# Kernel tuning notes

Measured on AMD Instinct MI355X. Metric: run time of the kernel, lower is better.

Reference implementation:

```python
import jax, jax.numpy as jnp
import numpy as np

EPS = 1e-16

def _householder_cascade(vectors):
    # vectors: [N, S, 1]
    v = vectors[..., 0]                                  # [N, S]
    outer = jnp.einsum('ns,nt->nst', v, v)               # [N, S, S]
    inner = jnp.sum(v * v, axis=-1)[:, None, None]       # [N, 1, 1]
    S = v.shape[-1]
    I = jnp.eye(S, dtype=vectors.dtype)
    hh = I[None] - 2.0 * outer / (inner + EPS)           # [N, S, S]
    # sequential left-to-right product: Q = H_0 @ H_1 @ ... @ H_{N-1}
    def step(Q, M):
        return Q @ M, None
    Q, _ = jax.lax.scan(step, I, hh)
    return Q

def setup_inputs() -> dict:
    key = jax.random.key(0)
    k1, k2 = jax.random.split(key)
    S, N, B = 256, 258, 65536
    vectors = jax.random.normal(k1, (N, S, 1), dtype=jnp.float32)
    vectors = vectors / jnp.linalg.norm(vectors, axis=1, keepdims=True)
    x = jax.random.normal(k2, (B, S), dtype=jnp.float32)
    return {"x": x, "vectors": vectors}

def reference(x, vectors):
    Q = _householder_cascade(vectors)   # [S, S]
    return x @ Q.T
```

## Files before the change

kernel.cpp:

```cpp
#include <hip/hip_runtime.h>


#define GLOAD_LDS16(g, l)                                                      \
  __builtin_amdgcn_global_load_lds(                                            \
      (const __attribute__((address_space(1))) void*)(g),                      \
      (__attribute__((address_space(3))) void*)(l), 16, 0, 0)

typedef __attribute__((ext_vector_type(8))) short bf16x8;
typedef __attribute__((ext_vector_type(4))) float f32x4;

__device__ __forceinline__ unsigned short f2bf_rne(float f) {
  unsigned u = __builtin_bit_cast(unsigned, f);
  return (unsigned short)((u + 0x7fffu + ((u >> 16) & 1u)) >> 16);
}

template <int CTRL>
__device__ __forceinline__ float dpp_add(float v) {
  int t = __builtin_amdgcn_update_dpp(0, __builtin_bit_cast(int, v), CTRL, 0xF,
                                      0xF, true);
  return v + __builtin_bit_cast(float, t);
}

__device__ __forceinline__ float dpp_sum16(float p) {
  p = dpp_add<0xB1>(p);
  p = dpp_add<0x4E>(p);
  p = dpp_add<0x124>(p);
  p = dpp_add<0x128>(p);
  return p;
}

__launch_bounds__(64, 1)
__global__ void hh_qchunk(const float* __restrict__ vecs,
                          float* __restrict__ Qc) {
  const int l = threadIdx.x;
  const int chunk = blockIdx.x >> 6;
  const int rg = blockIdx.x & 63;
  const int r = l >> 4;
  const int cl = l & 15;
  const int row = rg * 4 + r;
  const int col0 = cl * 16;
  const int brow = chunk * 129;

  __shared__ float cs[132];

  for (int n = r; n < 129; n += 4) {
    const f32x4* vp = (const f32x4*)(vecs + (long)(brow + n) * 256 + col0);
    float s = 0.f;
#pragma unroll
    for (int i = 0; i < 4; ++i) {
      f32x4 t = vp[i];
      s += t[0] * t[0] + t[1] * t[1] + t[2] * t[2] + t[3] * t[3];
    }
    s = dpp_sum16(s);
    if (cl == 0) cs[n] = 2.0f / (s + 1e-16f);
  }
  if (l < 3) cs[129 + l] = 0.f;
  __syncthreads();

  float q[16];
#pragma unroll
  for (int i = 0; i < 16; ++i) q[i] = (col0 + i == row) ? 1.f : 0.f;

  auto load16 = [&](float(&d)[16], int n) {
    int gr = brow + n;
    gr = gr > 257 ? 257 : gr;
    const float4* v = (const float4*)(vecs + (long)gr * 256 + col0);
#pragma unroll
    for (int i = 0; i < 4; ++i) {
      float4 t = v[i];
      d[4 * i] = t.x; d[4 * i + 1] = t.y; d[4 * i + 2] = t.z; d[4 * i + 3] = t.w;
    }
  };

  auto step = [&](const float(&a)[16], float cc) {
    float p0 = 0.f, p1 = 0.f, p2 = 0.f, p3 = 0.f;
#pragma unroll
    for (int e = 0; e < 4; ++e) {
      p0 = fmaf(q[e], a[e], p0);
      p1 = fmaf(q[4 + e], a[4 + e], p1);
      p2 = fmaf(q[8 + e], a[8 + e], p2);
      p3 = fmaf(q[12 + e], a[12 + e], p3);
    }
    const float p = dpp_sum16((p0 + p1) + (p2 + p3));
    const float s = cc * p;
#pragma unroll
    for (int k = 0; k < 16; ++k) q[k] = fmaf(-s, a[k], q[k]);
  };

  float A0[16], A1[16];
  load16(A0, 0);
  load16(A1, 1);
  float c0 = cs[0], c1 = cs[1];
  for (int n = 0; n < 128; n += 2) {
    const float cn0 = cs[n + 2], cn1 = cs[n + 3];
    step(A0, c0);
    load16(A0, n + 2);
    step(A1, c1);
    load16(A1, n + 3);
    c0 = cn0; c1 = cn1;
  }
  step(A0, c0);

  float4* out = (float4*)(Qc + (long)chunk * 65536 + row * 256 + col0);
#pragma unroll
  for (int i = 0; i < 4; ++i)
    out[i] = make_float4(q[4 * i], q[4 * i + 1], q[4 * i + 2], q[4 * i + 3]);
}

__launch_bounds__(256)
__global__ void hh_mm(const float* __restrict__ in,
                      unsigned short* __restrict__ outb) {
  const int t = blockIdx.x;
  const int ti = (t >> 3) * 32, tj = (t & 7) * 32;
  const int tid = threadIdx.x;
  const int tx = tid & 15, ty = tid >> 4;
  const float* A = in;
  const float* Bm = in + 65536;

  __shared__ float As[32][68];
  __shared__ float Bs[64][36];

  float acc00 = 0.f, acc01 = 0.f, acc10 = 0.f, acc11 = 0.f;

  for (int k0 = 0; k0 < 256; k0 += 64) {
#pragma unroll
    for (int u0 = 0; u0 < 2048; u0 += 1024) {
      int idx = u0 + tid * 4;
      int rr = idx >> 6, cc = idx & 63;
      *(float4*)&As[rr][cc] = *(const float4*)&A[(ti + rr) * 256 + k0 + cc];
      int kk = idx >> 5, jj = idx & 31;
      *(float4*)&Bs[kk][jj] = *(const float4*)&Bm[(k0 + kk) * 256 + tj + jj];
    }
    __syncthreads();
#pragma unroll 8
    for (int kk = 0; kk < 64; ++kk) {
      float a0 = As[2 * ty][kk], a1 = As[2 * ty + 1][kk];
      float b0 = Bs[kk][2 * tx], b1 = Bs[kk][2 * tx + 1];
      acc00 = fmaf(a0, b0, acc00);
      acc01 = fmaf(a0, b1, acc01);
      acc10 = fmaf(a1, b0, acc10);
      acc11 = fmaf(a1, b1, acc11);
    }
    __syncthreads();
  }

  const int gi = ti + 2 * ty, gj = tj + 2 * tx;
  outb[gi * 256 + gj] = f2bf_rne(acc00);
  outb[gi * 256 + gj + 1] = f2bf_rne(acc01);
  outb[(gi + 1) * 256 + gj] = f2bf_rne(acc10);
  outb[(gi + 1) * 256 + gj + 1] = f2bf_rne(acc11);
}

__launch_bounds__(512)
__global__ void hh_gemm(const float* __restrict__ X,
                        const unsigned short* __restrict__ Qb,
                        float* __restrict__ Y) {
  __shared__ __align__(128) char lds[65536];
  const int tid = threadIdx.x;
  const int lane = tid & 63;
  const int wid = tid >> 6;
  const int wm = wid >> 2;
  const int wn = wid & 3;
  const int fr = lane & 15;
  const int fg = lane >> 4;
  const long bm0 = (long)blockIdx.x * 128;

  auto stage = [&](int buf, int kt) {
#pragma unroll
    for (int r2 = 0; r2 < 2; ++r2) {
      int slot = r2 * 512 + tid;
      int row = slot >> 3, seg = slot & 7;
      int ps = seg ^ (row & 7);
      GLOAD_LDS16(X + (bm0 + row) * 256 + kt * 32 + ps * 4,
                  lds + buf * 16384 + slot * 16);
    }
#pragma unroll
    for (int r2 = 0; r2 < 2; ++r2) {
      int slot = r2 * 512 + tid;
      int row = slot >> 2, seg = slot & 3;
      int ps = seg ^ (row & 3);
      GLOAD_LDS16(Qb + row * 256 + kt * 32 + ps * 8,
                  lds + 32768 + buf * 16384 + slot * 16);
    }
  };

  f32x4 acc[4][4];
#pragma unroll
  for (int m = 0; m < 4; ++m)
#pragma unroll
    for (int n = 0; n < 4; ++n) acc[m][n] = (f32x4){0.f, 0.f, 0.f, 0.f};

  stage(0, 0);
  __syncthreads();

  for (int kt = 0; kt < 8; ++kt) {
    const int cur = kt & 1;
    if (kt < 7) stage(cur ^ 1, kt + 1);

    bf16x8 aF[4], bF[4];
#pragma unroll
    for (int m = 0; m < 4; ++m) {
      int row = wm * 64 + m * 16 + fr;
      int s0 = (2 * fg) ^ (row & 7);
      int s1 = (2 * fg + 1) ^ (row & 7);
      const f32x4 x0 = *(const f32x4*)(lds + cur * 16384 + row * 128 + s0 * 16);
      const f32x4 x1 = *(const f32x4*)(lds + cur * 16384 + row * 128 + s1 * 16);
      bf16x8 t;
      t[0] = (short)f2bf_rne(x0[0]);
      t[1] = (short)f2bf_rne(x0[1]);
      t[2] = (short)f2bf_rne(x0[2]);
      t[3] = (short)f2bf_rne(x0[3]);
      t[4] = (short)f2bf_rne(x1[0]);
      t[5] = (short)f2bf_rne(x1[1]);
      t[6] = (short)f2bf_rne(x1[2]);
      t[7] = (short)f2bf_rne(x1[3]);
      aF[m] = t;
    }
#pragma unroll
    for (int n = 0; n < 4; ++n) {
      int row = wn * 64 + n * 16 + fr;
      int ps = fg ^ (row & 3);
      bF[n] = *(const bf16x8*)(lds + 32768 + cur * 16384 + row * 64 + ps * 16);
    }
#pragma unroll
    for (int m = 0; m < 4; ++m)
#pragma unroll
      for (int n = 0; n < 4; ++n)
        acc[m][n] =
            __builtin_amdgcn_mfma_f32_16x16x32_bf16(aF[m], bF[n], acc[m][n], 0, 0, 0);
    __syncthreads();
  }

#pragma unroll
  for (int m = 0; m < 4; ++m)
#pragma unroll
    for (int n = 0; n < 4; ++n)
#pragma unroll
      for (int r = 0; r < 4; ++r) {
        long grow = bm0 + wm * 64 + m * 16 + fg * 4 + r;
        int gcol = wn * 64 + n * 16 + fr;
        Y[grow * 256 + gcol] = acc[m][n][r];
      }
}

extern "C" void kernel_launch(void* const* d_in, const int* in_sizes, int n_in,
                              void* d_out, int out_size, void* d_ws, size_t ws_size,
                              hipStream_t stream) {
  const float* x = (const float*)d_in[0];
  const float* vecs = (const float*)d_in[1];
  float* y = (float*)d_out;

  unsigned short* Qb = (unsigned short*)d_ws;
  float* Qc = (float*)d_out;

  hh_qchunk<<<128, 64, 0, stream>>>(vecs, Qc);
  hh_mm<<<64, 256, 0, stream>>>(Qc, Qb);
  hh_gemm<<<512, 512, 0, stream>>>(x, Qb, y);
}
```

Before: 74.56 us.

## Fuse Householder norm into step and deepen vector prefetch to four buffers

Drops the separate prologue that computed 2/(v·v+eps) for all 129 vectors into shared memory, along with its barrier. Each step now computes the squared norm alongside the dot product with a second DPP reduction. The vector load pipeline is deepened from two to four register buffers, and sched_barriers pin the order of step and load. This removes the serial prologue latency and hides more global load latency, at the cost of extra FMAs, an extra cross-lane reduction and a division per step, plus higher register pressure.

Result: faster. 65.84 us (-11.7%).

```diff
diff --git a/kernel.cpp b/kernel.cpp
--- a/kernel.cpp
+++ b/kernel.cpp
@@ -41,22 +41,6 @@
   const int col0 = cl * 16;
   const int brow = chunk * 129;
 
-  __shared__ float cs[132];
-
-  for (int n = r; n < 129; n += 4) {
-    const f32x4* vp = (const f32x4*)(vecs + (long)(brow + n) * 256 + col0);
-    float s = 0.f;
-#pragma unroll
-    for (int i = 0; i < 4; ++i) {
-      f32x4 t = vp[i];
-      s += t[0] * t[0] + t[1] * t[1] + t[2] * t[2] + t[3] * t[3];
-    }
-    s = dpp_sum16(s);
-    if (cl == 0) cs[n] = 2.0f / (s + 1e-16f);
-  }
-  if (l < 3) cs[129 + l] = 0.f;
-  __syncthreads();
-
   float q[16];
 #pragma unroll
   for (int i = 0; i < 16; ++i) q[i] = (col0 + i == row) ? 1.f : 0.f;
@@ -72,34 +56,42 @@
     }
   };
 
-  auto step = [&](const float(&a)[16], float cc) {
+  auto step = [&](const float(&a)[16]) {
     float p0 = 0.f, p1 = 0.f, p2 = 0.f, p3 = 0.f;
+    float s0 = 0.f, s1 = 0.f, s2 = 0.f, s3 = 0.f;
 #pragma unroll
     for (int e = 0; e < 4; ++e) {
       p0 = fmaf(q[e], a[e], p0);
       p1 = fmaf(q[4 + e], a[4 + e], p1);
       p2 = fmaf(q[8 + e], a[8 + e], p2);
       p3 = fmaf(q[12 + e], a[12 + e], p3);
+      s0 = fmaf(a[e], a[e], s0);
+      s1 = fmaf(a[4 + e], a[4 + e], s1);
+      s2 = fmaf(a[8 + e], a[8 + e], s2);
+      s3 = fmaf(a[12 + e], a[12 + e], s3);
     }
     const float p = dpp_sum16((p0 + p1) + (p2 + p3));
-    const float s = cc * p;
-#pragma unroll
-    for (int k = 0; k < 16; ++k) q[k] = fmaf(-s, a[k], q[k]);
+    const float s = dpp_sum16((s0 + s1) + (s2 + s3));
+    const float sc = (2.0f / (s + 1e-16f)) * p;
+#pragma unroll
+    for (int k = 0; k < 16; ++k) q[k] = fmaf(-sc, a[k], q[k]);
   };
 
-  float A0[16], A1[16];
-  load16(A0, 0);
-  load16(A1, 1);
-  float c0 = cs[0], c1 = cs[1];
-  for (int n = 0; n < 128; n += 2) {
-    const float cn0 = cs[n + 2], cn1 = cs[n + 3];
-    step(A0, c0);
-    load16(A0, n + 2);
-    step(A1, c1);
-    load16(A1, n + 3);
-    c0 = cn0; c1 = cn1;
+  float A0[16], A1[16], A2[16], A3[16];
+  load16(A0, 0); load16(A1, 1); load16(A2, 2); load16(A3, 3);
+
+  for (int t = 0; t < 32; ++t) {
+    const int n4 = 4 * t + 4;
+    step(A0); load16(A0, n4);
+    __builtin_amdgcn_sched_barrier(0);
+    step(A1); load16(A1, n4 + 1);
+    __builtin_amdgcn_sched_barrier(0);
+    step(A2); load16(A2, n4 + 2);
+    __builtin_amdgcn_sched_barrier(0);
+    step(A3); load16(A3, n4 + 3);
+    __builtin_amdgcn_sched_barrier(0);
   }
-  step(A0, c0);
+  step(A0);
 
   float4* out = (float4*)(Qc + (long)chunk * 65536 + row * 256 + col0);
 #pragma unroll
```
